# Optimization experiments

Hardware: AMD Instinct MI355X
Metric: run time of the kernel (lower is better)

## Reference

```python
import jax, jax.numpy as jnp
import numpy as np

B, S, H, DK, DV, D = 1024, 8, 16, 32, 32, 512


def setup_inputs() -> dict:
    key = jax.random.key(0)
    ks = jax.random.split(key, 12)
    s = 1.0 / np.sqrt(D)
    return {
        "Q": jax.random.normal(ks[0], (B, S, D), jnp.float32),
        "K": jax.random.normal(ks[1], (B, S, D), jnp.float32),
        "V": jax.random.normal(ks[2], (B, S, D), jnp.float32),
        "attn_mask": jax.random.bernoulli(ks[3], 0.2, (B, S, S)),
        "hyper": jax.random.normal(ks[4], (B, H * S * DK), jnp.float32),
        "Wq": jax.random.normal(ks[5], (H * DK, D), jnp.float32) * s,
        "bq": jnp.zeros((H * DK,), jnp.float32),
        "Wk": jax.random.normal(ks[6], (H * DK, D), jnp.float32) * s,
        "bk": jnp.zeros((H * DK,), jnp.float32),
        "Wv": jax.random.normal(ks[7], (H * DV, D), jnp.float32) * s,
        "bv": jnp.zeros((H * DV,), jnp.float32),
        "Wo": jax.random.normal(ks[8], (D, H * DV), jnp.float32) * s,
        "bo": jnp.zeros((D,), jnp.float32),
        "ln_g": jnp.ones((D,), jnp.float32),
        "ln_b": jnp.zeros((D,), jnp.float32),
    }


def reference(Q, K, V, attn_mask, hyper, Wq, bq, Wk, bk, Wv, bv, Wo, bo, ln_g, ln_b):
    # QKV projections -> [B, H, S, dk]
    q = (Q @ Wq.T + bq).reshape(B, S, H, DK).transpose(0, 2, 1, 3)
    k = (K @ Wk.T + bk).reshape(B, S, H, DK).transpose(0, 2, 1, 3)
    v = (V @ Wv.T + bv).reshape(B, S, H, DV).transpose(0, 2, 1, 3)
    # scaled dot-product attention with mask
    scores = jnp.einsum('bhqd,bhkd->bhqk', q, k) / np.sqrt(DK).astype(np.float32)
    scores = jnp.where(attn_mask[:, None, :, :], -1e9, scores)
    weights = jax.nn.softmax(scores, axis=-1)
    # hyper-gated AV
    context = jnp.einsum('bhqk,bhkd->bhqd', weights, v) * hyper.reshape(B, H, S, DK)
    context = context.transpose(0, 2, 1, 3).reshape(B, S, H * DV)
    # output projection + residual layernorm (eps=1e-5)
    out = context @ Wo.T + bo + Q
    mu = out.mean(axis=-1, keepdims=True)
    var = out.var(axis=-1, keepdims=True)
    out = (out - mu) * jax.lax.rsqrt(var + 1e-5) * ln_g + ln_b
    return (out, weights)
```

## Files before the change

kernel.cpp:

```cpp
#include <hip/hip_runtime.h>
#include <hip/hip_bf16.h>
#include <cstdint>

#define NB 1024
#define ND 512
#define NM 8192

typedef __attribute__((ext_vector_type(8))) short short8;
typedef __attribute__((ext_vector_type(8))) __bf16 bf16x8;
typedef __attribute__((ext_vector_type(4))) float f32x4;
typedef __attribute__((ext_vector_type(4))) unsigned short ushort4v;

__device__ __forceinline__ unsigned short f2bf(float f) {
  uint32_t x = __builtin_bit_cast(uint32_t, f);
  x += 0x7fffu + ((x >> 16) & 1u);
  return (unsigned short)(x >> 16);
}
__device__ __forceinline__ float bf2f(unsigned short u) {
  return __builtin_bit_cast(float, (uint32_t)u << 16);
}
__device__ __forceinline__ f32x4 mfma16(short8 a, short8 b, f32x4 c) {
  return __builtin_amdgcn_mfma_f32_16x16x32_bf16(
      __builtin_bit_cast(bf16x8, a), __builtin_bit_cast(bf16x8, b), c, 0, 0, 0);
}

__global__ __launch_bounds__(256) void convert_kernel(
    const float* __restrict__ Q, const float* __restrict__ K, const float* __restrict__ V,
    const float* __restrict__ Wq, const float* __restrict__ Wk, const float* __restrict__ Wv,
    const float* __restrict__ Wo,
    unsigned short* __restrict__ Qb, unsigned short* __restrict__ Kb,
    unsigned short* __restrict__ Vb, unsigned short* __restrict__ Wqb,
    unsigned short* __restrict__ Wkb, unsigned short* __restrict__ Wvb,
    unsigned short* __restrict__ Wob) {
  const int idx = blockIdx.x * 256 + threadIdx.x;
  const float* src;
  unsigned short* dst;
  int off;
  if (idx < 3 * 524288) {
    const int sel = idx >> 19, o = idx & 524287;
    src = sel == 0 ? Q : sel == 1 ? K : V;
    dst = sel == 0 ? Qb : sel == 1 ? Kb : Vb;
    off = o * 8;
  } else {
    const int w = idx - 3 * 524288;
    const int sel = w >> 15, o = w & 32767;
    src = sel == 0 ? Wq : sel == 1 ? Wk : sel == 2 ? Wv : Wo;
    dst = sel == 0 ? Wqb : sel == 1 ? Wkb : sel == 2 ? Wvb : Wob;
    off = o * 8;
  }
  const float4 a = ((const float4*)(src + off))[0];
  const float4 b = ((const float4*)(src + off))[1];
  short8 r;
  r[0] = (short)f2bf(a.x); r[1] = (short)f2bf(a.y);
  r[2] = (short)f2bf(a.z); r[3] = (short)f2bf(a.w);
  r[4] = (short)f2bf(b.x); r[5] = (short)f2bf(b.y);
  r[6] = (short)f2bf(b.z); r[7] = (short)f2bf(b.w);
  *(short8*)(dst + off) = r;
}

template <bool OUT_BF16>
__device__ __forceinline__ void gemm_tile(const unsigned short* __restrict__ A,
                                          const unsigned short* __restrict__ W,
                                          const float* __restrict__ bias,
                                          void* __restrict__ C, int mBase, int nBase) {
  __shared__ unsigned short As[128 * 64];
  __shared__ unsigned short Bs[128 * 64];
  const int tid = threadIdx.x;
  const int lane = tid & 63, wid = tid >> 6;
  const int wm = wid >> 2, wn = wid & 3;
  const int l15 = lane & 15, l4 = lane >> 4;
  f32x4 acc[4][2] = {};

  for (int kt = 0; kt < 8; ++kt) {
    const int kBase = kt * 64;
#pragma unroll
    for (int i = 0; i < 2; ++i) {
      const int Lb = i * 8192 + tid * 16;
      const int r = Lb >> 7;
      const int ce = (Lb & 127) >> 1;
      const int P = Lb ^ ((r & 7) << 4);
      const short8 av = *(const short8*)(A + (size_t)(mBase + r) * ND + kBase + ce);
      const short8 wv = *(const short8*)(W + (size_t)(nBase + r) * ND + kBase + ce);
      *(short8*)((char*)As + P) = av;
      *(short8*)((char*)Bs + P) = wv;
    }
    __syncthreads();
#pragma unroll
    for (int kk = 0; kk < 2; ++kk) {
      short8 af[4], bf4[2];
#pragma unroll
      for (int m = 0; m < 4; ++m) {
        const int r = wm * 64 + m * 16 + l15;
        const int Lb = r * 128 + kk * 64 + l4 * 16;
        af[m] = *(const short8*)((char*)As + (Lb ^ ((r & 7) << 4)));
      }
#pragma unroll
      for (int n = 0; n < 2; ++n) {
        const int r = wn * 32 + n * 16 + l15;
        const int Lb = r * 128 + kk * 64 + l4 * 16;
        bf4[n] = *(const short8*)((char*)Bs + (Lb ^ ((r & 7) << 4)));
      }
#pragma unroll
      for (int m = 0; m < 4; ++m)
#pragma unroll
        for (int n = 0; n < 2; ++n)
          acc[m][n] = mfma16(af[m], bf4[n], acc[m][n]);
    }
    __syncthreads();
  }

#pragma unroll
  for (int m = 0; m < 4; ++m)
#pragma unroll
    for (int n = 0; n < 2; ++n) {
      const int gn = nBase + wn * 32 + n * 16 + l15;
      const float bb = bias ? bias[gn] : 0.f;
#pragma unroll
      for (int r4 = 0; r4 < 4; ++r4) {
        const int gm = mBase + wm * 64 + m * 16 + l4 * 4 + r4;
        const float val = acc[m][n][r4] + bb;
        if (OUT_BF16)
          ((unsigned short*)C)[(size_t)gm * ND + gn] = f2bf(val);
        else
          ((float*)C)[(size_t)gm * ND + gn] = val;
      }
    }
}

__global__ __launch_bounds__(512) void gemm_qkv(
    const unsigned short* __restrict__ Qb, const unsigned short* __restrict__ Kb,
    const unsigned short* __restrict__ Vb, const unsigned short* __restrict__ Wqb,
    const unsigned short* __restrict__ Wkb, const unsigned short* __restrict__ Wvb,
    const float* __restrict__ bq, const float* __restrict__ bk,
    const float* __restrict__ bv, unsigned short* __restrict__ qo,
    unsigned short* __restrict__ ko, unsigned short* __restrict__ vo) {
  const int nb = blockIdx.x;
  const int seg = nb >> 2, nloc = nb & 3;
  const unsigned short* A = seg == 0 ? Qb : seg == 1 ? Kb : Vb;
  const unsigned short* W = seg == 0 ? Wqb : seg == 1 ? Wkb : Wvb;
  const float* bias = seg == 0 ? bq : seg == 1 ? bk : bv;
  unsigned short* C = seg == 0 ? qo : seg == 1 ? ko : vo;
  gemm_tile<true>(A, W, bias, C, blockIdx.y * 128, nloc * 128);
}

__global__ __launch_bounds__(512) void gemm_wo(const unsigned short* __restrict__ ctx,
                                               const unsigned short* __restrict__ Wob,
                                               float* __restrict__ out) {
  gemm_tile<false>(ctx, Wob, nullptr, out, blockIdx.y * 128, blockIdx.x * 128);
}

__global__ __launch_bounds__(256) void attn_kernel(
    const unsigned short* __restrict__ q, const unsigned short* __restrict__ k,
    const unsigned short* __restrict__ v, const int* __restrict__ mask,
    const float* __restrict__ hyper, float* __restrict__ wout,
    unsigned short* __restrict__ ctx) {
  const int tid = threadIdx.x;
  const int wid = tid >> 6, lane = tid & 63;
  const int t = blockIdx.x * 4 + wid;
  const int b = t >> 4, h = t & 15;
  const int i = lane >> 3, j = lane & 7;

  const unsigned short* qrow = q + (size_t)(b * 8 + i) * ND + h * 32;
  const unsigned short* krow = k + (size_t)(b * 8 + j) * ND + h * 32;
  float dot = 0.f;
#pragma unroll
  for (int c = 0; c < 4; ++c) {
    const short8 qv = ((const short8*)qrow)[c];
    const short8 kv = ((const short8*)krow)[c];
#pragma unroll
    for (int e = 0; e < 8; ++e)
      dot += bf2f((unsigned short)qv[e]) * bf2f((unsigned short)kv[e]);
  }
  float score = dot * 0.17677669529663687f;
  if (mask[b * 64 + i * 8 + j]) score = -1e9f;

  float mx = score;
#pragma unroll
  for (int o = 4; o; o >>= 1) mx = fmaxf(mx, __shfl_xor(mx, o, 8));
  const float e = __expf(score - mx);
  float sm = e;
#pragma unroll
  for (int o = 4; o; o >>= 1) sm += __shfl_xor(sm, o, 8);
  const float w = e / sm;
  wout[(size_t)t * 64 + lane] = w;

  const int d0 = (lane & 7) * 4;
  float c0 = 0, c1 = 0, c2 = 0, c3 = 0;
#pragma unroll
  for (int jj = 0; jj < 8; ++jj) {
    const float wj = __shfl(w, jj, 8);
    const ushort4v vv = *(const ushort4v*)(v + (size_t)(b * 8 + jj) * ND + h * 32 + d0);
    c0 += wj * bf2f(vv[0]); c1 += wj * bf2f(vv[1]);
    c2 += wj * bf2f(vv[2]); c3 += wj * bf2f(vv[3]);
  }
  const float4 hv = *(const float4*)(hyper + (size_t)b * 4096 + h * 256 + i * 32 + d0);
  ushort4v co;
  co[0] = f2bf(c0 * hv.x); co[1] = f2bf(c1 * hv.y);
  co[2] = f2bf(c2 * hv.z); co[3] = f2bf(c3 * hv.w);
  *(ushort4v*)(ctx + (size_t)(b * 8 + i) * ND + h * 32 + d0) = co;
}

__global__ __launch_bounds__(256) void ln_kernel(float* __restrict__ io,
                                                 const float* __restrict__ Qin,
                                                 const float* __restrict__ bo,
                                                 const float* __restrict__ g,
                                                 const float* __restrict__ be) {
  const int tid = threadIdx.x, wid = tid >> 6, lane = tid & 63;
  const size_t row = (size_t)blockIdx.x * 4 + wid;
  float* prow = io + row * ND + lane * 8;
  const float* qrow = Qin + row * ND + lane * 8;
  float4 x0 = ((float4*)prow)[0], x1 = ((float4*)prow)[1];
  const float4 q0 = ((const float4*)qrow)[0], q1 = ((const float4*)qrow)[1];
  const float4 b0 = ((const float4*)(bo + lane * 8))[0];
  const float4 b1 = ((const float4*)(bo + lane * 8))[1];
  x0.x += q0.x + b0.x; x0.y += q0.y + b0.y; x0.z += q0.z + b0.z; x0.w += q0.w + b0.w;
  x1.x += q1.x + b1.x; x1.y += q1.y + b1.y; x1.z += q1.z + b1.z; x1.w += q1.w + b1.w;
  float s = x0.x + x0.y + x0.z + x0.w + x1.x + x1.y + x1.z + x1.w;
  float sq = x0.x * x0.x + x0.y * x0.y + x0.z * x0.z + x0.w * x0.w +
             x1.x * x1.x + x1.y * x1.y + x1.z * x1.z + x1.w * x1.w;
#pragma unroll
  for (int o = 32; o; o >>= 1) {
    s += __shfl_xor(s, o, 64);
    sq += __shfl_xor(sq, o, 64);
  }
  const float mu = s * (1.f / 512.f);
  const float inv = rsqrtf(sq * (1.f / 512.f) - mu * mu + 1e-5f);
  const float4 g0 = ((const float4*)(g + lane * 8))[0];
  const float4 g1 = ((const float4*)(g + lane * 8))[1];
  const float4 e0 = ((const float4*)(be + lane * 8))[0];
  const float4 e1 = ((const float4*)(be + lane * 8))[1];
  float4 o0, o1;
  o0.x = (x0.x - mu) * inv * g0.x + e0.x; o0.y = (x0.y - mu) * inv * g0.y + e0.y;
  o0.z = (x0.z - mu) * inv * g0.z + e0.z; o0.w = (x0.w - mu) * inv * g0.w + e0.w;
  o1.x = (x1.x - mu) * inv * g1.x + e1.x; o1.y = (x1.y - mu) * inv * g1.y + e1.y;
  o1.z = (x1.z - mu) * inv * g1.z + e1.z; o1.w = (x1.w - mu) * inv * g1.w + e1.w;
  ((float4*)prow)[0] = o0;
  ((float4*)prow)[1] = o1;
}

extern "C" void kernel_launch(void* const* d_in, const int* in_sizes, int n_in,
                              void* d_out, int out_size, void* d_ws, size_t ws_size,
                              hipStream_t stream) {
  const float* Q = (const float*)d_in[0];
  const float* K = (const float*)d_in[1];
  const float* V = (const float*)d_in[2];
  const int* msk = (const int*)d_in[3];
  const float* hyper = (const float*)d_in[4];
  const float* Wq = (const float*)d_in[5];
  const float* bq = (const float*)d_in[6];
  const float* Wk = (const float*)d_in[7];
  const float* bk = (const float*)d_in[8];
  const float* Wv = (const float*)d_in[9];
  const float* bv = (const float*)d_in[10];
  const float* Wo = (const float*)d_in[11];
  const float* bo = (const float*)d_in[12];
  const float* lg = (const float*)d_in[13];
  const float* lb = (const float*)d_in[14];

  float* out = (float*)d_out;
  float* wout = out + (size_t)NM * ND;

  const size_t MAT = (size_t)NM * ND;
  unsigned short* Qb = (unsigned short*)d_ws;
  unsigned short* Kb = Qb + MAT;
  unsigned short* Vb = Kb + MAT;
  unsigned short* qb = Vb + MAT;
  unsigned short* kb = qb + MAT;
  unsigned short* vb = kb + MAT;
  unsigned short* ctxb = vb + MAT;
  unsigned short* Wqb = ctxb + MAT;
  unsigned short* Wkb = Wqb + (size_t)ND * ND;
  unsigned short* Wvb = Wkb + (size_t)ND * ND;
  unsigned short* Wob = Wvb + (size_t)ND * ND;

  convert_kernel<<<6656, 256, 0, stream>>>(Q, K, V, Wq, Wk, Wv, Wo,
                                           Qb, Kb, Vb, Wqb, Wkb, Wvb, Wob);
  gemm_qkv<<<dim3(12, 64), 512, 0, stream>>>(Qb, Kb, Vb, Wqb, Wkb, Wvb,
                                             bq, bk, bv, qb, kb, vb);
  attn_kernel<<<4096, 256, 0, stream>>>(qb, kb, vb, msk, hyper, wout, ctxb);
  gemm_wo<<<dim3(4, 64), 512, 0, stream>>>(ctxb, Wob, out);
  ln_kernel<<<2048, 256, 0, stream>>>(out, Q, bo, lg, lb);
}
```

Measured before the change: 80.14 us.

## Use direct global-to-LDS loads, XCD-aware block remap, fuse residual into Wo GEMM

Replaces the register-staged, XOR-swizzled shared-memory tile loads in the GEMM with global_load_lds direct copies into an unswizzled row-major LDS layout. Both GEMM launches become 1D grids with a block-index remap that groups neighbouring tiles on the same XCD for L2 reuse. The output bias and Q residual add move from the layernorm kernel into the Wo GEMM epilogue, which removes one read pass over Q there. Dropping the swizzle risks LDS bank conflicts on the fragment reads.

```diff
diff --git a/kernel.cpp b/kernel.cpp
--- a/kernel.cpp
+++ b/kernel.cpp
@@ -22,6 +22,11 @@
 __device__ __forceinline__ f32x4 mfma16(short8 a, short8 b, f32x4 c) {
   return __builtin_amdgcn_mfma_f32_16x16x32_bf16(
       __builtin_bit_cast(bf16x8, a), __builtin_bit_cast(bf16x8, b), c, 0, 0, 0);
+}
+__device__ __forceinline__ void gl_lds16(const unsigned short* g, unsigned short* lds) {
+  __builtin_amdgcn_global_load_lds(
+      (const __attribute__((address_space(1))) unsigned int*)g,
+      (__attribute__((address_space(3))) unsigned int*)lds, 16, 0, 0);
 }
 
 __global__ __launch_bounds__(256) void convert_kernel(
@@ -58,10 +63,11 @@
   *(short8*)(dst + off) = r;
 }
 
-template <bool OUT_BF16>
+template <int MODE>
 __device__ __forceinline__ void gemm_tile(const unsigned short* __restrict__ A,
                                           const unsigned short* __restrict__ W,
                                           const float* __restrict__ bias,
+                                          const float* __restrict__ resid,
                                           void* __restrict__ C, int mBase, int nBase) {
   __shared__ unsigned short As[128 * 64];
   __shared__ unsigned short Bs[128 * 64];
@@ -69,37 +75,28 @@
   const int lane = tid & 63, wid = tid >> 6;
   const int wm = wid >> 2, wn = wid & 3;
   const int l15 = lane & 15, l4 = lane >> 4;
+  const int srow = wid * 16;
+  const int lrow = lane >> 3, lcol = (lane & 7) * 8;
   f32x4 acc[4][2] = {};
 
   for (int kt = 0; kt < 8; ++kt) {
     const int kBase = kt * 64;
 #pragma unroll
     for (int i = 0; i < 2; ++i) {
-      const int Lb = i * 8192 + tid * 16;
-      const int r = Lb >> 7;
-      const int ce = (Lb & 127) >> 1;
-      const int P = Lb ^ ((r & 7) << 4);
-      const short8 av = *(const short8*)(A + (size_t)(mBase + r) * ND + kBase + ce);
-      const short8 wv = *(const short8*)(W + (size_t)(nBase + r) * ND + kBase + ce);
-      *(short8*)((char*)As + P) = av;
-      *(short8*)((char*)Bs + P) = wv;
+      const int r0 = srow + i * 8;
+      gl_lds16(A + (size_t)(mBase + r0 + lrow) * ND + kBase + lcol, &As[r0 * 64]);
+      gl_lds16(W + (size_t)(nBase + r0 + lrow) * ND + kBase + lcol, &Bs[r0 * 64]);
     }
     __syncthreads();
 #pragma unroll
     for (int kk = 0; kk < 2; ++kk) {
       short8 af[4], bf4[2];
 #pragma unroll
-      for (int m = 0; m < 4; ++m) {
-        const int r = wm * 64 + m * 16 + l15;
-        const int Lb = r * 128 + kk * 64 + l4 * 16;
-        af[m] = *(const short8*)((char*)As + (Lb ^ ((r & 7) << 4)));
-      }
-#pragma unroll
-      for (int n = 0; n < 2; ++n) {
-        const int r = wn * 32 + n * 16 + l15;
-        const int Lb = r * 128 + kk * 64 + l4 * 16;
-        bf4[n] = *(const short8*)((char*)Bs + (Lb ^ ((r & 7) << 4)));
-      }
+      for (int m = 0; m < 4; ++m)
+        af[m] = *(const short8*)&As[(wm * 64 + m * 16 + l15) * 64 + kk * 32 + l4 * 8];
+#pragma unroll
+      for (int n = 0; n < 2; ++n)
+        bf4[n] = *(const short8*)&Bs[(wn * 32 + n * 16 + l15) * 64 + kk * 32 + l4 * 8];
 #pragma unroll
       for (int m = 0; m < 4; ++m)
 #pragma unroll
@@ -118,11 +115,13 @@
 #pragma unroll
       for (int r4 = 0; r4 < 4; ++r4) {
         const int gm = mBase + wm * 64 + m * 16 + l4 * 4 + r4;
-        const float val = acc[m][n][r4] + bb;
-        if (OUT_BF16)
+        float val = acc[m][n][r4] + bb;
+        if (MODE == 0) {
           ((unsigned short*)C)[(size_t)gm * ND + gn] = f2bf(val);
-        else
+        } else {
+          val += resid[(size_t)gm * ND + gn];
           ((float*)C)[(size_t)gm * ND + gn] = val;
+        }
       }
     }
 }
@@ -134,19 +133,26 @@
     const float* __restrict__ bq, const float* __restrict__ bk,
     const float* __restrict__ bv, unsigned short* __restrict__ qo,
     unsigned short* __restrict__ ko, unsigned short* __restrict__ vo) {
-  const int nb = blockIdx.x;
-  const int seg = nb >> 2, nloc = nb & 3;
+  const int bid = blockIdx.x;
+  const int lid = (bid & 7) * 96 + (bid >> 3);
+  const int by = lid / 12, bx = lid % 12;
+  const int seg = bx >> 2, nloc = bx & 3;
   const unsigned short* A = seg == 0 ? Qb : seg == 1 ? Kb : Vb;
   const unsigned short* W = seg == 0 ? Wqb : seg == 1 ? Wkb : Wvb;
   const float* bias = seg == 0 ? bq : seg == 1 ? bk : bv;
   unsigned short* C = seg == 0 ? qo : seg == 1 ? ko : vo;
-  gemm_tile<true>(A, W, bias, C, blockIdx.y * 128, nloc * 128);
+  gemm_tile<0>(A, W, bias, nullptr, C, by * 128, nloc * 128);
 }
 
 __global__ __launch_bounds__(512) void gemm_wo(const unsigned short* __restrict__ ctx,
                                                const unsigned short* __restrict__ Wob,
+                                               const float* __restrict__ bo,
+                                               const float* __restrict__ Qres,
                                                float* __restrict__ out) {
-  gemm_tile<false>(ctx, Wob, nullptr, out, blockIdx.y * 128, blockIdx.x * 128);
+  const int bid = blockIdx.x;
+  const int lid = (bid & 7) * 32 + (bid >> 3);
+  const int by = lid >> 2, bx = lid & 3;
+  gemm_tile<1>(ctx, Wob, bo, Qres, out, by * 128, bx * 128);
 }
 
 __global__ __launch_bounds__(256) void attn_kernel(
@@ -201,20 +207,12 @@
 }
 
 __global__ __launch_bounds__(256) void ln_kernel(float* __restrict__ io,
-                                                 const float* __restrict__ Qin,
-                                                 const float* __restrict__ bo,
                                                  const float* __restrict__ g,
                                                  const float* __restrict__ be) {
   const int tid = threadIdx.x, wid = tid >> 6, lane = tid & 63;
   const size_t row = (size_t)blockIdx.x * 4 + wid;
   float* prow = io + row * ND + lane * 8;
-  const float* qrow = Qin + row * ND + lane * 8;
   float4 x0 = ((float4*)prow)[0], x1 = ((float4*)prow)[1];
-  const float4 q0 = ((const float4*)qrow)[0], q1 = ((const float4*)qrow)[1];
-  const float4 b0 = ((const float4*)(bo + lane * 8))[0];
-  const float4 b1 = ((const float4*)(bo + lane * 8))[1];
-  x0.x += q0.x + b0.x; x0.y += q0.y + b0.y; x0.z += q0.z + b0.z; x0.w += q0.w + b0.w;
-  x1.x += q1.x + b1.x; x1.y += q1.y + b1.y; x1.z += q1.z + b1.z; x1.w += q1.w + b1.w;
   float s = x0.x + x0.y + x0.z + x0.w + x1.x + x1.y + x1.z + x1.w;
   float sq = x0.x * x0.x + x0.y * x0.y + x0.z * x0.z + x0.w * x0.w +
              x1.x * x1.x + x1.y * x1.y + x1.z * x1.z + x1.w * x1.w;
@@ -275,9 +273,9 @@
 
   convert_kernel<<<6656, 256, 0, stream>>>(Q, K, V, Wq, Wk, Wv, Wo,
                                            Qb, Kb, Vb, Wqb, Wkb, Wvb, Wob);
-  gemm_qkv<<<dim3(12, 64), 512, 0, stream>>>(Qb, Kb, Vb, Wqb, Wkb, Wvb,
-                                             bq, bk, bv, qb, kb, vb);
+  gemm_qkv<<<768, 512, 0, stream>>>(Qb, Kb, Vb, Wqb, Wkb, Wvb,
+                                    bq, bk, bv, qb, kb, vb);
   attn_kernel<<<4096, 256, 0, stream>>>(qb, kb, vb, msk, hyper, wout, ctxb);
-  gemm_wo<<<dim3(4, 64), 512, 0, stream>>>(ctxb, Wob, out);
-  ln_kernel<<<2048, 256, 0, stream>>>(out, Q, bo, lg, lb);
-}
+  gemm_wo<<<256, 512, 0, stream>>>(ctxb, Wob, bo, Q, out);
+  ln_kernel<<<2048, 256, 0, stream>>>(out, lg, lb);
+}
```

Result: slower. 84.14 us (+5.0%).
